# Optimization experiments

Measured on AMD Instinct MI355X. Metric: run time of the kernel, lower is better.

The kernel has to match this reference:

```python
import jax, jax.numpy as jnp
import numpy as np

C = 256
CQK = C // 8  # 32

def setup_inputs() -> dict:
    key = jax.random.key(0)
    ks = jax.random.split(key, 9)
    B, H, W = 4, 64, 64
    s = 0.02
    return {
        "x": jax.random.normal(ks[0], (B, C, W, H), jnp.float32),
        "y": jax.random.normal(ks[1], (B, C, W, H), jnp.float32),
        "Wq": jax.random.normal(ks[2], (CQK, C), jnp.float32) * s,
        "bq": jax.random.normal(ks[3], (CQK,), jnp.float32) * s,
        "Wk": jax.random.normal(ks[4], (CQK, C), jnp.float32) * s,
        "bk": jax.random.normal(ks[5], (CQK,), jnp.float32) * s,
        "Wv": jax.random.normal(ks[6], (C, C), jnp.float32) * s,
        "bv": jax.random.normal(ks[7], (C,), jnp.float32) * s,
        "gamma": jnp.zeros((1,), jnp.float32) + 0.1,  # nonzero so output depends on attention
    }

def reference(x, y, Wq, bq, Wk, bk, Wv, bv, gamma):
    B, Cc, Wd, Hd = x.shape
    N = Wd * Hd
    xf = x.reshape(B, Cc, N)  # [B,C,N]
    yf = y.reshape(B, Cc, N)
    # 1x1 convs == channel matmuls
    q = jnp.einsum('dc,bcn->bnd', Wq, xf) + bq  # [B,N,CQK]
    k = jnp.einsum('dc,bcn->bdn', Wk, yf) + bk[None, :, None]  # [B,CQK,N]
    v = jnp.einsum('ec,bcn->ben', Wv, yf) + bv[None, :, None]  # [B,C,N]
    energy = jnp.einsum('bnd,bdm->bnm', q, k)  # [B,N,N]
    attn = jax.nn.softmax(energy, axis=-1)
    out = jnp.einsum('bem,bnm->ben', v, attn)  # [B,C,N]
    out = out.reshape(B, Cc, Wd, Hd)
    return gamma * out + x
```

## Files before the change

kernel.cpp:

```cpp
#include <hip/hip_runtime.h>
#include <hip/hip_bf16.h>
#include <stdint.h>

#define B_   4
#define C_   256
#define CQK_ 32
#define N_   4096

typedef float f32x4  __attribute__((ext_vector_type(4)));
typedef short bf16x8 __attribute__((ext_vector_type(8)));
typedef unsigned uint4v __attribute__((ext_vector_type(4)));

__device__ __forceinline__ unsigned short f2bf(float f) {
    unsigned u = __builtin_bit_cast(unsigned, f);
    u += 0x7FFFu + ((u >> 16) & 1u);
    return (unsigned short)(u >> 16);
}
__device__ __forceinline__ unsigned pack2(float a, float b) {
    return (unsigned)f2bf(a) | ((unsigned)f2bf(b) << 16);
}

__device__ __forceinline__ size_t vfrag_off(int b, int e, int m) {
    return ((((size_t)b * 128 + (m >> 5)) * 16 + (e >> 4)) * 64
            + (size_t)((m >> 3) & 3) * 16 + (e & 15)) * 8 + (m & 7);
}

__global__ __launch_bounds__(256) void wconv_kernel(
        const float* __restrict__ Wq, const float* __restrict__ Wk,
        const float* __restrict__ Wv,
        unsigned short* __restrict__ Wqb, unsigned short* __restrict__ Wkb,
        unsigned short* __restrict__ Wvb) {
    for (int p = blockIdx.x * 256 + threadIdx.x; p < 40960; p += 64 * 256) {
        const float* s; unsigned short* d; int off;
        if (p < 4096)      { s = Wq; d = Wqb; off = p; }
        else if (p < 8192) { s = Wk; d = Wkb; off = p - 4096; }
        else               { s = Wv; d = Wvb; off = p - 8192; }
        *(unsigned*)(d + off * 2) = pack2(s[off * 2], s[off * 2 + 1]);
    }
}

__global__ __launch_bounds__(256) void proj_gemm(
        const float* __restrict__ x, const float* __restrict__ y,
        const unsigned short* __restrict__ Wqb, const unsigned short* __restrict__ Wkb,
        const unsigned short* __restrict__ Wvb,
        const float* __restrict__ bq, const float* __restrict__ bk,
        const float* __restrict__ bv,
        unsigned short* __restrict__ qf, unsigned short* __restrict__ kf,
        unsigned short* __restrict__ vf) {
    __shared__ char xlds[64 * 512];
    __shared__ char ylds[64 * 512];
    const int tid = threadIdx.x, w = tid >> 6, l = tid & 63;
    const int lr = l & 15, lg = l >> 4;
    const int gid = blockIdx.x;
    const int b  = (gid >> 1) & 3;
    const int n0 = ((((gid >> 3) << 1) | (gid & 1))) * 64;

    {
        const int j = l & 7;
        const float* spx = x + (size_t)b * C_ * N_ + n0 + l;
        const float* spy = y + (size_t)b * C_ * N_ + n0 + l;
#pragma unroll
        for (int gl = 0; gl < 8; ++gl) {
            const int c8 = w * 64 + gl * 8;
            const int slot = (gl + j) & 7;
            uint4v px, py;
#pragma unroll
            for (int t = 0; t < 4; ++t) {
                px[t] = pack2(spx[(size_t)(c8 + 2 * t) * N_], spx[(size_t)(c8 + 2 * t + 1) * N_]);
                py[t] = pack2(spy[(size_t)(c8 + 2 * t) * N_], spy[(size_t)(c8 + 2 * t + 1) * N_]);
            }
            *(uint4v*)(xlds + l * 512 + w * 128 + slot * 16) = px;
            *(uint4v*)(ylds + l * 512 + w * 128 + slot * 16) = py;
        }
    }
    __syncthreads();

#define AFRAG(LDS, ROW, G)                                                     \
    (*(const bf16x8*)((LDS) + (ROW) * 512 + ((G) >> 3) * 128                   \
                      + ((((G) & 7) + ((ROW) & 7)) & 7) * 16))

    f32x4 accV[4][4];
    f32x4 accQ[4];
#pragma unroll
    for (int e = 0; e < 4; ++e)
#pragma unroll
        for (int m = 0; m < 4; ++m) accV[e][m] = (f32x4){0.f, 0.f, 0.f, 0.f};
#pragma unroll
    for (int m = 0; m < 4; ++m) accQ[m] = (f32x4){0.f, 0.f, 0.f, 0.f};

    const unsigned short* __restrict__ Wqk = (w < 2) ? Wqb : Wkb;
    const int d0 = (w & 1) * 16;

#pragma unroll
    for (int ks = 0; ks < 8; ++ks) {
        const int c0 = ks * 32 + lg * 8;
        const int g  = ks * 4 + lg;
        bf16x8 aY[4], aS[4];
#pragma unroll
        for (int mb = 0; mb < 4; ++mb) aY[mb] = AFRAG(ylds, mb * 16 + lr, g);
        if (w < 2) {
#pragma unroll
            for (int mb = 0; mb < 4; ++mb) aS[mb] = AFRAG(xlds, mb * 16 + lr, g);
        } else {
#pragma unroll
            for (int mb = 0; mb < 4; ++mb) aS[mb] = aY[mb];
        }
        bf16x8 bV[4];
#pragma unroll
        for (int eb = 0; eb < 4; ++eb)
            bV[eb] = *(const bf16x8*)(Wvb + (size_t)(w * 64 + eb * 16 + lr) * C_ + c0);
        const bf16x8 bQ = *(const bf16x8*)(Wqk + (size_t)(d0 + lr) * C_ + c0);
#pragma unroll
        for (int eb = 0; eb < 4; ++eb)
#pragma unroll
            for (int mb = 0; mb < 4; ++mb)
                accV[eb][mb] = __builtin_amdgcn_mfma_f32_16x16x32_bf16(
                    aY[mb], bV[eb], accV[eb][mb], 0, 0, 0);
#pragma unroll
        for (int mb = 0; mb < 4; ++mb)
            accQ[mb] = __builtin_amdgcn_mfma_f32_16x16x32_bf16(aS[mb], bQ, accQ[mb], 0, 0, 0);
    }
#undef AFRAG

#pragma unroll
    for (int eb = 0; eb < 4; ++eb) {
        const int e = w * 64 + eb * 16 + lr;
        const float bve = bv[e];
#pragma unroll
        for (int mb = 0; mb < 4; ++mb) {
            const size_t off = vfrag_off(b, e, n0 + mb * 16 + lg * 4);
            unsigned* p = (unsigned*)(vf + off);
            p[0] = pack2(accV[eb][mb][0] + bve, accV[eb][mb][1] + bve);
            p[1] = pack2(accV[eb][mb][2] + bve, accV[eb][mb][3] + bve);
        }
    }
    const float bqv = ((w < 2) ? bq : bk)[d0 + lr];
    unsigned short* __restrict__ dqk = (w < 2) ? qf : kf;
#pragma unroll
    for (int mb = 0; mb < 4; ++mb)
#pragma unroll
        for (int r = 0; r < 4; ++r) {
            const int n = n0 + mb * 16 + lg * 4 + r;
            dqk[((size_t)b * N_ + n) * CQK_ + d0 + lr] = f2bf(accQ[mb][r] + bqv);
        }
}

__global__ __launch_bounds__(512, 2) void attn_kernel(
        const unsigned short* __restrict__ qf, const unsigned short* __restrict__ kf,
        const unsigned short* __restrict__ vf, const float* __restrict__ x,
        const float* __restrict__ gamma, float* __restrict__ out) {
    __shared__ char plds[2][64 * 272];
    __shared__ float oslab[2][64][128];
    __shared__ float cLs[8][64];
    __shared__ float cLt[64];
    const int tid = threadIdx.x, w = tid >> 6, l = tid & 63;
    const int lr = l & 15, lg = l >> 4;
    const int gid = blockIdx.x;
    const int b  = (gid >> 1) & 3;
    const int q0 = ((((gid >> 3) << 1) | (gid & 1))) * 64;
    const int eh = w >> 2, ksw = w & 3;

    bf16x8 qfr[4];
#pragma unroll
    for (int qblk = 0; qblk < 4; ++qblk)
        qfr[qblk] = *(const bf16x8*)(
            qf + ((size_t)b * N_ + q0 + qblk * 16 + lr) * CQK_ + lg * 8);

    f32x4 acc[4][8];
#pragma unroll
    for (int i = 0; i < 4; ++i)
#pragma unroll
        for (int j = 0; j < 8; ++j) acc[i][j] = (f32x4){0.f, 0.f, 0.f, 0.f};
    float Lacc[4] = {0.f, 0.f, 0.f, 0.f};

    const unsigned short* kbase = kf + ((size_t)b * N_ + w * 16 + lr) * CQK_ + lg * 8;

#define PREF_K(T, K)                                                           \
    K = *(const bf16x8*)(kbase + (size_t)(((T) & 31) * 128) * CQK_);

#define PREF_V(T)                                                              \
    {                                                                          \
        const int t_ = (T) & 31;                                               \
        _Pragma("unroll")                                                      \
        for (int ebi_ = 0; ebi_ < 8; ++ebi_)                                   \
            vV[ebi_] = *(const bf16x8*)(                                       \
                vf + ((size_t)((b * 128 + t_ * 4 + ksw) * 16 + eh * 8 + ebi_)) \
                         * 512 + l * 8);                                       \
    }

#define BODY(T, K)                                                             \
    {                                                                          \
        f32x4 e4_[4];                                                          \
        _Pragma("unroll")                                                      \
        for (int qblk = 0; qblk < 4; ++qblk)                                   \
            e4_[qblk] = __builtin_amdgcn_mfma_f32_16x16x32_bf16(               \
                K, qfr[qblk], (f32x4){0.f, 0.f, 0.f, 0.f}, 0, 0, 0);           \
        char* pw_ = plds[(T) & 1];                                             \
        const int m2_ = w * 16 + lg * 4;                                       \
        _Pragma("unroll")                                                      \
        for (int qblk = 0; qblk < 4; ++qblk) {                                 \
            const float p0 = __expf(e4_[qblk][0]);                             \
            const float p1 = __expf(e4_[qblk][1]);                             \
            const float p2 = __expf(e4_[qblk][2]);                             \
            const float p3 = __expf(e4_[qblk][3]);                             \
            Lacc[qblk] += (p0 + p1) + (p2 + p3);                               \
            unsigned u0, u1;                                                   \
            asm("v_cvt_pk_bf16_f32 %0, %1, %2" : "=v"(u0) : "v"(p0), "v"(p1)); \
            asm("v_cvt_pk_bf16_f32 %0, %1, %2" : "=v"(u1) : "v"(p2), "v"(p3)); \
            const int q_ = qblk * 16 + lr;                                     \
            const int byte_ = q_ * 272 + ((m2_ >> 3) << 4) + (m2_ & 7) * 2;    \
            *(unsigned long long*)(pw_ + byte_) =                              \
                (unsigned long long)u0 | ((unsigned long long)u1 << 32);       \
        }                                                                      \
        asm volatile("s_waitcnt lgkmcnt(0)" ::: "memory");                     \
        __builtin_amdgcn_s_barrier();                                          \
        asm volatile("" ::: "memory");                                         \
        PREF_K((T) + 2, K);                                                    \
        __builtin_amdgcn_s_setprio(1);                                         \
        _Pragma("unroll")                                                      \
        for (int qblk = 0; qblk < 4; ++qblk) {                                 \
            const int q_ = qblk * 16 + lr;                                     \
            const bf16x8 pa_ = *(const bf16x8*)(                               \
                pw_ + q_ * 272 + ((ksw * 4 + lg) << 4));                       \
            _Pragma("unroll")                                                  \
            for (int ebi_ = 0; ebi_ < 8; ++ebi_)                               \
                acc[qblk][ebi_] = __builtin_amdgcn_mfma_f32_16x16x32_bf16(     \
                    pa_, vV[ebi_], acc[qblk][ebi_], 0, 0, 0);                  \
        }                                                                      \
        __builtin_amdgcn_s_setprio(0);                                         \
        PREF_V((T) + 1);                  \
    }

    bf16x8 kA, kB, vV[8];
    PREF_K(0, kA);
    PREF_K(1, kB);
    PREF_V(0);

    for (int kt = 0; kt < 32; kt += 2) {
        BODY(kt, kA);
        BODY(kt + 1, kB);
    }
#undef PREF_K
#undef PREF_V
#undef BODY

#pragma unroll
    for (int qblk = 0; qblk < 4; ++qblk) {
        Lacc[qblk] += __shfl_xor(Lacc[qblk], 16);
        Lacc[qblk] += __shfl_xor(Lacc[qblk], 32);
    }
    if (l < 16) {
#pragma unroll
        for (int qblk = 0; qblk < 4; ++qblk) cLs[w][qblk * 16 + lr] = Lacc[qblk];
    }
    __syncthreads();
    if (tid < 64) {
        float s = 0.f;
#pragma unroll
        for (int w2 = 0; w2 < 8; ++w2) s += cLs[w2][tid];
        cLt[tid] = 1.0f / s;
    }
    __syncthreads();

#pragma unroll
    for (int round = 3; round > 0; --round) {
        if (ksw == round) {
#pragma unroll
            for (int qblk = 0; qblk < 4; ++qblk)
#pragma unroll
                for (int ebi = 0; ebi < 8; ++ebi)
#pragma unroll
                    for (int r = 0; r < 4; ++r)
                        oslab[eh][qblk * 16 + lg * 4 + r][ebi * 16 + lr] = acc[qblk][ebi][r];
        }
        __syncthreads();
        if (ksw == round - 1) {
#pragma unroll
            for (int qblk = 0; qblk < 4; ++qblk)
#pragma unroll
                for (int ebi = 0; ebi < 8; ++ebi)
#pragma unroll
                    for (int r = 0; r < 4; ++r)
                        acc[qblk][ebi][r] += oslab[eh][qblk * 16 + lg * 4 + r][ebi * 16 + lr];
        }
        __syncthreads();
    }
    if (ksw == 0) {
#pragma unroll
        for (int qblk = 0; qblk < 4; ++qblk)
#pragma unroll
            for (int ebi = 0; ebi < 8; ++ebi)
#pragma unroll
                for (int r = 0; r < 4; ++r)
                    oslab[eh][qblk * 16 + lg * 4 + r][ebi * 16 + lr] = acc[qblk][ebi][r];
    }
    __syncthreads();

    const float g = gamma[0];
#pragma unroll
    for (int qblk = 0; qblk < 4; ++qblk) {
        float rI[4];
#pragma unroll
        for (int r = 0; r < 4; ++r) rI[r] = cLt[qblk * 16 + lg * 4 + r];
        const int nb = q0 + qblk * 16 + lg * 4;
#pragma unroll
        for (int ebi = 0; ebi < 2; ++ebi) {
            const int e = (w * 2 + ebi) * 16 + lr;
            const size_t idx = ((size_t)b * C_ + e) * N_ + nb;
            const f32x4 xv = *(const f32x4*)(x + idx);
            f32x4 ov;
#pragma unroll
            for (int r = 0; r < 4; ++r) {
                const float val = oslab[e >> 7][qblk * 16 + lg * 4 + r][e & 127];
                ov[r] = g * val * rI[r] + xv[r];
            }
            *(f32x4*)(out + idx) = ov;
        }
    }
}

extern "C" void kernel_launch(void* const* d_in, const int* in_sizes, int n_in,
                              void* d_out, int out_size, void* d_ws, size_t ws_size,
                              hipStream_t stream) {
    (void)in_sizes; (void)n_in; (void)out_size; (void)ws_size;
    const float* x     = (const float*)d_in[0];
    const float* y     = (const float*)d_in[1];
    const float* Wq    = (const float*)d_in[2];
    const float* bq    = (const float*)d_in[3];
    const float* Wk    = (const float*)d_in[4];
    const float* bk    = (const float*)d_in[5];
    const float* Wv    = (const float*)d_in[6];
    const float* bv    = (const float*)d_in[7];
    const float* gamma = (const float*)d_in[8];
    float* out = (float*)d_out;

    unsigned short* qf  = (unsigned short*)d_ws;
    unsigned short* kf  = qf + (size_t)B_ * N_ * CQK_;
    unsigned short* vf  = kf + (size_t)B_ * N_ * CQK_;
    unsigned short* Wqb = vf + (size_t)B_ * N_ * C_;
    unsigned short* Wkb = Wqb + CQK_ * C_;
    unsigned short* Wvb = Wkb + CQK_ * C_;

    wconv_kernel<<<dim3(64), 256, 0, stream>>>(Wq, Wk, Wv, Wqb, Wkb, Wvb);
    proj_gemm<<<dim3(256), 256, 0, stream>>>(x, y, Wqb, Wkb, Wvb, bq, bk, bv, qf, kf, vf);
    attn_kernel<<<dim3(256), 512, 0, stream>>>(qf, kf, vf, x, gamma, out);
}
```

Baseline: 70.04 us.

## Halve attention query tile to 32 and double grid with 2-way key split

The attention kernel now handles 32 queries per block instead of 64 and launches twice as many blocks. Each wave covers a quarter of the output channels and half of each key tile, so the cross-wave reduction is a single 2-way add instead of a 4-round chain. Register and LDS use drop, and the launch bound asks for 4 blocks per SM instead of 2, to improve occupancy and latency hiding. The cost is that K and V tiles are reused across half as many queries, which doubles total K/V reads from cache.

```diff
diff --git a/kernel.cpp b/kernel.cpp
--- a/kernel.cpp
+++ b/kernel.cpp
@@ -145,33 +145,33 @@
         }
 }
 
-__global__ __launch_bounds__(512, 2) void attn_kernel(
+__global__ __launch_bounds__(512, 4) void attn_kernel(
         const unsigned short* __restrict__ qf, const unsigned short* __restrict__ kf,
         const unsigned short* __restrict__ vf, const float* __restrict__ x,
         const float* __restrict__ gamma, float* __restrict__ out) {
-    __shared__ char plds[2][64 * 272];
-    __shared__ float oslab[2][64][128];
-    __shared__ float cLs[8][64];
-    __shared__ float cLt[64];
+    __shared__ char plds[2][32 * 272];
+    __shared__ float oslab[32][256];
+    __shared__ float cLs[8][32];
+    __shared__ float cLt[32];
     const int tid = threadIdx.x, w = tid >> 6, l = tid & 63;
     const int lr = l & 15, lg = l >> 4;
     const int gid = blockIdx.x;
     const int b  = (gid >> 1) & 3;
-    const int q0 = ((((gid >> 3) << 1) | (gid & 1))) * 64;
-    const int eh = w >> 2, ksw = w & 3;
-
-    bf16x8 qfr[4];
-#pragma unroll
-    for (int qblk = 0; qblk < 4; ++qblk)
+    const int q0 = ((((gid >> 3) << 1) | (gid & 1))) * 32;
+    const int eq = w >> 1, ksh = w & 1;
+
+    bf16x8 qfr[2];
+#pragma unroll
+    for (int qblk = 0; qblk < 2; ++qblk)
         qfr[qblk] = *(const bf16x8*)(
             qf + ((size_t)b * N_ + q0 + qblk * 16 + lr) * CQK_ + lg * 8);
 
-    f32x4 acc[4][8];
-#pragma unroll
-    for (int i = 0; i < 4; ++i)
-#pragma unroll
-        for (int j = 0; j < 8; ++j) acc[i][j] = (f32x4){0.f, 0.f, 0.f, 0.f};
-    float Lacc[4] = {0.f, 0.f, 0.f, 0.f};
+    f32x4 acc[2][4];
+#pragma unroll
+    for (int i = 0; i < 2; ++i)
+#pragma unroll
+        for (int j = 0; j < 4; ++j) acc[i][j] = (f32x4){0.f, 0.f, 0.f, 0.f};
+    float Lacc[2] = {0.f, 0.f};
 
     const unsigned short* kbase = kf + ((size_t)b * N_ + w * 16 + lr) * CQK_ + lg * 8;
 
@@ -182,23 +182,25 @@
     {                                                                          \
         const int t_ = (T) & 31;                                               \
         _Pragma("unroll")                                                      \
-        for (int ebi_ = 0; ebi_ < 8; ++ebi_)                                   \
-            vV[ebi_] = *(const bf16x8*)(                                       \
-                vf + ((size_t)((b * 128 + t_ * 4 + ksw) * 16 + eh * 8 + ebi_)) \
-                         * 512 + l * 8);                                       \
+        for (int ci_ = 0; ci_ < 2; ++ci_)                                      \
+            _Pragma("unroll")                                                  \
+            for (int ebi_ = 0; ebi_ < 4; ++ebi_)                               \
+                vV[ci_][ebi_] = *(const bf16x8*)(                              \
+                    vf + ((size_t)((b * 128 + t_ * 4 + ksh * 2 + ci_) * 16     \
+                                   + eq * 4 + ebi_)) * 512 + l * 8);           \
     }
 
 #define BODY(T, K)                                                             \
     {                                                                          \
-        f32x4 e4_[4];                                                          \
+        f32x4 e4_[2];                                                          \
         _Pragma("unroll")                                                      \
-        for (int qblk = 0; qblk < 4; ++qblk)                                   \
+        for (int qblk = 0; qblk < 2; ++qblk)                                   \
             e4_[qblk] = __builtin_amdgcn_mfma_f32_16x16x32_bf16(               \
                 K, qfr[qblk], (f32x4){0.f, 0.f, 0.f, 0.f}, 0, 0, 0);           \
         char* pw_ = plds[(T) & 1];                                             \
         const int m2_ = w * 16 + lg * 4;                                       \
         _Pragma("unroll")                                                      \
-        for (int qblk = 0; qblk < 4; ++qblk) {                                 \
+        for (int qblk = 0; qblk < 2; ++qblk) {                                 \
             const float p0 = __expf(e4_[qblk][0]);                             \
             const float p1 = __expf(e4_[qblk][1]);                             \
             const float p2 = __expf(e4_[qblk][2]);                             \
@@ -218,20 +220,22 @@
         PREF_K((T) + 2, K);                                                    \
         __builtin_amdgcn_s_setprio(1);                                         \
         _Pragma("unroll")                                                      \
-        for (int qblk = 0; qblk < 4; ++qblk) {                                 \
-            const int q_ = qblk * 16 + lr;                                     \
-            const bf16x8 pa_ = *(const bf16x8*)(                               \
-                pw_ + q_ * 272 + ((ksw * 4 + lg) << 4));                       \
+        for (int ci_ = 0; ci_ < 2; ++ci_)                                      \
             _Pragma("unroll")                                                  \
-            for (int ebi_ = 0; ebi_ < 8; ++ebi_)                               \
-                acc[qblk][ebi_] = __builtin_amdgcn_mfma_f32_16x16x32_bf16(     \
-                    pa_, vV[ebi_], acc[qblk][ebi_], 0, 0, 0);                  \
-        }                                                                      \
+            for (int qblk = 0; qblk < 2; ++qblk) {                             \
+                const int q_ = qblk * 16 + lr;                                 \
+                const bf16x8 pa_ = *(const bf16x8*)(                           \
+                    pw_ + q_ * 272 + (((ksh * 2 + ci_) * 4 + lg) << 4));       \
+                _Pragma("unroll")                                              \
+                for (int ebi_ = 0; ebi_ < 4; ++ebi_)                           \
+                    acc[qblk][ebi_] = __builtin_amdgcn_mfma_f32_16x16x32_bf16( \
+                        pa_, vV[ci_][ebi_], acc[qblk][ebi_], 0, 0, 0);         \
+            }                                                                  \
         __builtin_amdgcn_s_setprio(0);                                         \
         PREF_V((T) + 1);                  \
     }
 
-    bf16x8 kA, kB, vV[8];
+    bf16x8 kA, kB, vV[2][4];
     PREF_K(0, kA);
     PREF_K(1, kB);
     PREF_V(0);
@@ -245,60 +249,50 @@
 #undef BODY
 
 #pragma unroll
-    for (int qblk = 0; qblk < 4; ++qblk) {
+    for (int qblk = 0; qblk < 2; ++qblk) {
         Lacc[qblk] += __shfl_xor(Lacc[qblk], 16);
         Lacc[qblk] += __shfl_xor(Lacc[qblk], 32);
     }
     if (l < 16) {
 #pragma unroll
-        for (int qblk = 0; qblk < 4; ++qblk) cLs[w][qblk * 16 + lr] = Lacc[qblk];
-    }
-    __syncthreads();
-    if (tid < 64) {
+        for (int qblk = 0; qblk < 2; ++qblk) cLs[w][qblk * 16 + lr] = Lacc[qblk];
+    }
+    __syncthreads();
+    if (tid < 32) {
         float s = 0.f;
 #pragma unroll
         for (int w2 = 0; w2 < 8; ++w2) s += cLs[w2][tid];
         cLt[tid] = 1.0f / s;
     }
-    __syncthreads();
-
-#pragma unroll
-    for (int round = 3; round > 0; --round) {
-        if (ksw == round) {
-#pragma unroll
-            for (int qblk = 0; qblk < 4; ++qblk)
-#pragma unroll
-                for (int ebi = 0; ebi < 8; ++ebi)
-#pragma unroll
-                    for (int r = 0; r < 4; ++r)
-                        oslab[eh][qblk * 16 + lg * 4 + r][ebi * 16 + lr] = acc[qblk][ebi][r];
-        }
-        __syncthreads();
-        if (ksw == round - 1) {
-#pragma unroll
-            for (int qblk = 0; qblk < 4; ++qblk)
-#pragma unroll
-                for (int ebi = 0; ebi < 8; ++ebi)
-#pragma unroll
-                    for (int r = 0; r < 4; ++r)
-                        acc[qblk][ebi][r] += oslab[eh][qblk * 16 + lg * 4 + r][ebi * 16 + lr];
-        }
-        __syncthreads();
-    }
-    if (ksw == 0) {
-#pragma unroll
-        for (int qblk = 0; qblk < 4; ++qblk)
-#pragma unroll
-            for (int ebi = 0; ebi < 8; ++ebi)
+
+    __syncthreads();
+    if (ksh == 1) {
+#pragma unroll
+        for (int qblk = 0; qblk < 2; ++qblk)
+#pragma unroll
+            for (int ebi = 0; ebi < 4; ++ebi)
 #pragma unroll
                 for (int r = 0; r < 4; ++r)
-                    oslab[eh][qblk * 16 + lg * 4 + r][ebi * 16 + lr] = acc[qblk][ebi][r];
+                    oslab[qblk * 16 + lg * 4 + r][(eq * 4 + ebi) * 16 + lr] = acc[qblk][ebi][r];
+    }
+    __syncthreads();
+    if (ksh == 0) {
+#pragma unroll
+        for (int qblk = 0; qblk < 2; ++qblk)
+#pragma unroll
+            for (int ebi = 0; ebi < 4; ++ebi)
+#pragma unroll
+                for (int r = 0; r < 4; ++r) {
+                    const int qr = qblk * 16 + lg * 4 + r;
+                    const int e  = (eq * 4 + ebi) * 16 + lr;
+                    oslab[qr][e] += acc[qblk][ebi][r];
+                }
     }
     __syncthreads();
 
     const float g = gamma[0];
 #pragma unroll
-    for (int qblk = 0; qblk < 4; ++qblk) {
+    for (int qblk = 0; qblk < 2; ++qblk) {
         float rI[4];
 #pragma unroll
         for (int r = 0; r < 4; ++r) rI[r] = cLt[qblk * 16 + lg * 4 + r];
@@ -310,10 +304,8 @@
             const f32x4 xv = *(const f32x4*)(x + idx);
             f32x4 ov;
 #pragma unroll
-            for (int r = 0; r < 4; ++r) {
-                const float val = oslab[e >> 7][qblk * 16 + lg * 4 + r][e & 127];
-                ov[r] = g * val * rI[r] + xv[r];
-            }
+            for (int r = 0; r < 4; ++r)
+                ov[r] = g * oslab[qblk * 16 + lg * 4 + r][e] * rI[r] + xv[r];
             *(f32x4*)(out + idx) = ov;
         }
     }
@@ -343,5 +335,5 @@
 
     wconv_kernel<<<dim3(64), 256, 0, stream>>>(Wq, Wk, Wv, Wqb, Wkb, Wvb);
     proj_gemm<<<dim3(256), 256, 0, stream>>>(x, y, Wqb, Wkb, Wvb, bq, bk, bv, qf, kf, vf);
-    attn_kernel<<<dim3(256), 512, 0, stream>>>(qf, kf, vf, x, gamma, out);
-}
+    attn_kernel<<<dim3(512), 512, 0, stream>>>(qf, kf, vf, x, gamma, out);
+}
```

Result: slower. 78.85 us (+12.6%).
